# Performance work log

Hardware: AMD Instinct MI355X
Metric: run time of the kernel (lower is better)

## Reference

```python
import jax, jax.numpy as jnp
import numpy as np

B, T, C, H, L, V = 8, 512, 512, 8, 2, 512
DH = C // H
SCALE = 1.0 / np.sqrt(DH)


def _ln(x, g, b):
    mu = jnp.mean(x, -1, keepdims=True)
    var = jnp.mean((x - mu) ** 2, -1, keepdims=True)
    return (x - mu) * jax.lax.rsqrt(var + 1e-5) * g + b


def setup_inputs() -> dict:
    key = jax.random.key(0)
    ks = jax.random.split(key, 16)
    f = lambda k, shape: jax.random.normal(k, shape, jnp.float32) * 0.02
    return {
        "idx": jax.random.randint(ks[0], (B, T), 0, 4),
        "tok_emb": f(ks[1], (4, C)),
        "pos_emb": f(ks[2], (T, C)),
        "ln1_g": jnp.ones((L, C)), "ln1_b": jnp.zeros((L, C)),
        "Wq": f(ks[3], (L, C, C)), "bq": jnp.zeros((L, C)),
        "Wk": f(ks[4], (L, C, C)), "bk": jnp.zeros((L, C)),
        "Wv": f(ks[5], (L, C, C)), "bv": jnp.zeros((L, C)),
        "Wp": f(ks[6], (L, C, C)), "bp": jnp.zeros((L, C)),
        "ln2_g": jnp.ones((L, C)), "ln2_b": jnp.zeros((L, C)),
        "W1": f(ks[7], (L, C, 4 * C)), "b1": jnp.zeros((L, 4 * C)),
        "W2": f(ks[8], (L, 4 * C, C)), "b2": jnp.zeros((L, C)),
        "lnf_g": jnp.ones((C,)), "lnf_b": jnp.zeros((C,)),
        "Whead": f(ks[9], (C, V)),
        "steps": 4,
    }


def _block(x, p):
    (l1g, l1b, wq, bq, wk, bk, wv, bv, wp, bp,
     l2g, l2b, w1, b1, w2, b2) = p
    # attention (mask buffer is all ones in the original -> full attention)
    xn = _ln(x, l1g, l1b)
    q = (xn @ wq + bq).reshape(B, T, H, DH)
    k = (xn @ wk + bk).reshape(B, T, H, DH)
    v = (xn @ wv + bv).reshape(B, T, H, DH)
    att = jnp.einsum('bqhd,bkhd->bhqk', q, k) * SCALE
    att = jax.nn.softmax(att, axis=-1)
    y = jnp.einsum('bhqk,bkhd->bqhd', att, v).reshape(B, T, C)
    x = x + y @ wp + bp
    # MLP with exact (erf) GELU, matching torch nn.GELU default
    h = jax.nn.gelu(_ln(x, l2g, l2b) @ w1 + b1, approximate=False)
    return x + h @ w2 + b2


def reference(idx, tok_emb, pos_emb, ln1_g, ln1_b, Wq, bq, Wk, bk, Wv, bv,
              Wp, bp, ln2_g, ln2_b, W1, b1, W2, b2, lnf_g, lnf_b, Whead,
              steps):
    params = (ln1_g, ln1_b, Wq, bq, Wk, bk, Wv, bv, Wp, bp,
              ln2_g, ln2_b, W1, b1, W2, b2)
    x = tok_emb[idx] + pos_emb[None, :, :]

    def run_blocks(x):
        def step(x, p):
            return _block(x, p), None
        x, _ = jax.lax.scan(step, x, params)
        return x

    for _ in range(steps):  # recurrent application of the whole stack
        x = run_blocks(x)
    x = _ln(x, lnf_g, lnf_b)
    return x @ Whead  # logits [B, T, V]
```

## Files before the change

kernel.cpp:

```cpp
#include <hip/hip_runtime.h>
#include <hip/hip_bf16.h>
#include <math.h>

#define BB 8
#define TT 512
#define CC 512
#define HH 8
#define DH 64
#define LL 2
#define VV 512
#define NSTEPS 4
#define BT (BB*TT)
#define FF (4*CC)

typedef unsigned short u16;
typedef __bf16 bf16x8 __attribute__((ext_vector_type(8)));
typedef float f32x4 __attribute__((ext_vector_type(4)));
typedef u16 u16x8 __attribute__((ext_vector_type(8)));

static __device__ __forceinline__ u16 f2bf(float f) {
    unsigned int u = __float_as_uint(f);
    unsigned int r = (u + 0x7fffu + ((u >> 16) & 1u)) >> 16;
    return (u16)r;
}

static __device__ __forceinline__ void async16(const void* g, void* l) {
    __builtin_amdgcn_global_load_lds((__attribute__((address_space(1))) void*)g,
                                     (__attribute__((address_space(3))) void*)l, 16, 0, 0);
}

static __device__ __forceinline__ int swzp(int r) { return (r ^ (r >> 2)) & 7; }

__global__ void embed_kernel(const int* __restrict__ idx, const float* __restrict__ tok,
                             const float* __restrict__ pos, float* __restrict__ x) {
    int bt = blockIdx.x;
    int t  = threadIdx.x;
    int token = idx[bt];
    int posrow = bt % TT;
    x[(size_t)bt*CC + t]       = tok[token*CC + t]       + pos[posrow*CC + t];
    x[(size_t)bt*CC + t + 256] = tok[token*CC + t + 256] + pos[posrow*CC + t + 256];
}

__global__ __launch_bounds__(256)
void ln_kernel(const float* __restrict__ x, const float* __restrict__ g,
               const float* __restrict__ b, u16* __restrict__ out) {
    int wid = threadIdx.x >> 6, lane = threadIdx.x & 63;
    int row = blockIdx.x * 4 + wid;
    const float* xr = x + (size_t)row * CC;
    f32x4 v0 = ((const f32x4*)xr)[lane*2];
    f32x4 v1 = ((const f32x4*)xr)[lane*2 + 1];
    float s = 0.f, sq = 0.f;
#pragma unroll
    for (int j = 0; j < 4; j++) {
        s += v0[j] + v1[j];
        sq += v0[j]*v0[j] + v1[j]*v1[j];
    }
#pragma unroll
    for (int off = 1; off < 64; off <<= 1) { s += __shfl_xor(s, off); sq += __shfl_xor(sq, off); }
    float mean = s * (1.0f / CC);
    float var  = sq * (1.0f / CC) - mean * mean;
    float inv  = rsqrtf(var + 1e-5f);
    f32x4 g0 = ((const f32x4*)g)[lane*2], g1 = ((const f32x4*)g)[lane*2 + 1];
    f32x4 b0 = ((const f32x4*)b)[lane*2], b1 = ((const f32x4*)b)[lane*2 + 1];
    u16x8 o;
#pragma unroll
    for (int j = 0; j < 4; j++) o[j]     = f2bf((v0[j] - mean) * inv * g0[j] + b0[j]);
#pragma unroll
    for (int j = 0; j < 4; j++) o[4 + j] = f2bf((v1[j] - mean) * inv * g1[j] + b1[j]);
    *(u16x8*)&out[(size_t)row*CC + lane*8] = o;
}

__global__ __launch_bounds__(256)
void cast_all_kernel(const float* __restrict__ Wq, const float* __restrict__ Wk,
                     const float* __restrict__ Wv, const float* __restrict__ Wp,
                     const float* __restrict__ W1, const float* __restrict__ W2,
                     const float* __restrict__ Wh,
                     u16* w_qkvt, u16* w_pt, u16* w_1t, u16* w_2t, u16* w_ht) {
    int bid = blockIdx.x;
    const float* src; u16* dst; int K, N, i0, j0;
    const size_t wcc = (size_t)CC*CC, wcf = (size_t)CC*FF;
    if (bid < 1536) {
        int l = bid / 768, r = bid % 768;
        if (r < 256) {
            int m = r / 64, t = r % 64;
            K = CC; N = CC;
            i0 = (t / 8) * 64; j0 = (t % 8) * 64;
            if      (m == 0) { src = Wq + l*wcc; dst = w_qkvt + (size_t)l*3*wcc; }
            else if (m == 1) { src = Wk + l*wcc; dst = w_qkvt + (size_t)l*3*wcc + wcc; }
            else if (m == 2) { src = Wv + l*wcc; dst = w_qkvt + (size_t)l*3*wcc + 2*wcc; }
            else             { src = Wp + l*wcc; dst = w_pt + (size_t)l*wcc; }
        } else if (r < 512) {
            int t = r - 256;
            K = CC; N = FF;
            i0 = (t / 32) * 64; j0 = (t % 32) * 64;
            src = W1 + l*wcf; dst = w_1t + (size_t)l*wcf;
        } else {
            int t = r - 512;
            K = FF; N = CC;
            i0 = (t / 8) * 64; j0 = (t % 8) * 64;
            src = W2 + l*wcf; dst = w_2t + (size_t)l*wcf;
        }
    } else {
        int t = bid - 1536;
        K = CC; N = CC;
        i0 = (t / 8) * 64; j0 = (t % 8) * 64;
        src = Wh; dst = w_ht;
    }
    __shared__ float tile[64][65];
    int tt = threadIdx.x;
    int rr = tt >> 2, cg = (tt & 3) * 16;
#pragma unroll
    for (int i = 0; i < 16; i++)
        tile[rr][cg + i] = src[(size_t)(i0 + rr) * N + j0 + cg + i];
    __syncthreads();
#pragma unroll
    for (int i = 0; i < 16; i++)
        dst[(size_t)(j0 + rr) * K + i0 + cg + i] = f2bf(tile[cg + i][rr]);
}

template<int BM, int BN, int THREADS, int WROWS, int WCOLS, int EPI>
__global__ __launch_bounds__(THREADS, 6)
void gemm_bt_kernel(const u16* __restrict__ A, const u16* __restrict__ Bt,
                    int N, int K,
                    const float* __restrict__ bias, const float* __restrict__ biask,
                    const float* __restrict__ biasv,
                    float* outf, u16* outq, u16* outk, u16* outvt) {
    constexpr int WTM = BM / WROWS, WTN = BN / WCOLS;
    constexpr int TM = WTM / 16, TN = WTN / 16;
    static_assert(THREADS / 4 == 2 * BM, "A staged in exactly one call");
    static_assert(THREADS == WROWS * WCOLS * 64, "wave grid");
    __shared__ u16 lds_a[2][2][BM][32];
    __shared__ u16 lds_b[2][2][BN][32];
    int tid = threadIdx.x;
    int wid = tid >> 6, lane = tid & 63;
    int quad = lane >> 4, l15 = lane & 15;
    int wm = (wid % WROWS) * WTM, wn = (wid / WROWS) * WTN;

    int NBN = N / BN;
    int lin = blockIdx.x;
    int x8 = lin & 7, slot = lin >> 3;
    int bn = slot % NBN;
    int bm = (slot / NBN) * 8 + x8;

    const int fr = tid >> 2;
    const int c2 = tid & 3;
    const size_t a0 = (size_t)bm * BM, b0 = (size_t)bn * BN;

    auto stage = [&](int buf, int kt) {
        {
            int ks2 = fr / BM, row = fr % BM;
            int g = (ks2 * 4 + c2) ^ swzp(row);
            async16(&A[(a0 + row) * K + kt + g * 8], &lds_a[buf][ks2][row][c2 * 8]);
        }
#pragma unroll
        for (int i = 0; i < (2 * BN) / (THREADS / 4); i++) {
            int f = fr + i * (THREADS / 4);
            int ks2 = f / BN, row = f % BN;
            int g = (ks2 * 4 + c2) ^ swzp(row);
            async16(&Bt[(b0 + row) * K + kt + g * 8], &lds_b[buf][ks2][row][c2 * 8]);
        }
    };

    f32x4 zero = {0.f, 0.f, 0.f, 0.f};
    f32x4 acc[TM][TN];
#pragma unroll
    for (int mi = 0; mi < TM; mi++)
#pragma unroll
        for (int ni = 0; ni < TN; ni++) acc[mi][ni] = zero;

    stage(0, 0);
    __syncthreads();
    const int NKT = K / 64;
    for (int kt = 0; kt < NKT; kt++) {
        int cur = kt & 1;
        if (kt + 1 < NKT) stage(cur ^ 1, (kt + 1) * 64);
#pragma unroll
        for (int ks = 0; ks < 2; ks++) {
            bf16x8 af[TM], bfr[TN];
#pragma unroll
            for (int mi = 0; mi < TM; mi++) {
                int row = wm + mi*16 + l15;
                int lc = (ks*4 + quad) ^ swzp(row);
                af[mi] = *(const bf16x8*)&lds_a[cur][lc >> 2][row][(lc & 3) * 8];
            }
#pragma unroll
            for (int ni = 0; ni < TN; ni++) {
                int row = wn + ni*16 + l15;
                int lc = (ks*4 + quad) ^ swzp(row);
                bfr[ni] = *(const bf16x8*)&lds_b[cur][lc >> 2][row][(lc & 3) * 8];
            }
#pragma unroll
            for (int mi = 0; mi < TM; mi++)
#pragma unroll
                for (int ni = 0; ni < TN; ni++)
                    acc[mi][ni] = __builtin_amdgcn_mfma_f32_16x16x32_bf16(af[mi], bfr[ni], acc[mi][ni], 0, 0, 0);
        }
        __syncthreads();
    }

#pragma unroll
    for (int mi = 0; mi < TM; mi++)
#pragma unroll
        for (int ni = 0; ni < TN; ni++)
#pragma unroll
            for (int i = 0; i < 4; i++) {
                int row = bm*BM + wm + mi*16 + quad*4 + i;
                int col = bn*BN + wn + ni*16 + l15;
                float v = acc[mi][ni][i];
                if (EPI == 0) {
                    int region = col >> 9, cl = col & 511;
                    if (region == 0) {
                        v = (v + bias[cl]) * 0.125f;
                        outq[(size_t)row*512 + cl] = f2bf(v);
                    } else if (region == 1) {
                        v += biask[cl];
                        outk[(size_t)row*512 + cl] = f2bf(v);
                    } else {
                        v += biasv[cl];
                        int bb = row >> 9, tpos = row & 511, hh = cl >> 6, dh = cl & 63;
                        outvt[(((size_t)(bb*8 + hh)*64 + dh) << 9) + tpos] = f2bf(v);
                    }
                } else if (EPI == 1) {
                    size_t idx2 = (size_t)row * N + col;
                    v += bias[col] + outf[idx2];
                    outf[idx2] = v;
                } else if (EPI == 2) {
                    v += bias[col];
                    v = 0.5f * v * (1.0f + erff(v * 0.70710678118654752f));
                    outq[(size_t)row * N + col] = f2bf(v);
                } else {
                    outf[(size_t)row * N + col] = v;
                }
            }
}

__global__ __launch_bounds__(256)
void attn_mfma_kernel(const u16* __restrict__ q, const u16* __restrict__ k,
                      const u16* __restrict__ vt, u16* __restrict__ y) {
    __shared__ u16 lq[64][64];
    __shared__ u16 lk[2][64][64];
    __shared__ u16 lv[2][64][64];
    __shared__ u16 lp[4][16][72];
    int qt = blockIdx.x, h = blockIdx.y, b = blockIdx.z;
    int tid = threadIdx.x;
    int wid = tid >> 6, lane = tid & 63;
    int quad = lane >> 4, l15 = lane & 15;
    const int sr = tid >> 3;
    const int sc = (tid & 7) * 8;
    const int gsc = (((tid & 7) ^ swzp(sr)) << 3);

    auto stageKV = [&](int buf, int kt) {
#pragma unroll
        for (int c = 0; c < 2; c++) {
            async16(&k[(size_t)(b*TT + kt*64 + c*32 + sr)*CC + h*DH + gsc], &lk[buf][c*32 + sr][sc]);
            async16(&vt[((size_t)((b*HH + h)*DH + c*32 + sr))*TT + kt*64 + gsc], &lv[buf][c*32 + sr][sc]);
        }
    };

#pragma unroll
    for (int c = 0; c < 2; c++)
        async16(&q[(size_t)(b*TT + qt*64 + c*32 + sr)*CC + h*DH + gsc], &lq[c*32 + sr][sc]);
    stageKV(0, 0);
    __syncthreads();

    f32x4 zero = {0.f, 0.f, 0.f, 0.f};
    f32x4 acc_o[4];
    float m_st[4], l_st[4];
#pragma unroll
    for (int i = 0; i < 4; i++) { m_st[i] = -INFINITY; l_st[i] = 0.f; }
#pragma unroll
    for (int ni = 0; ni < 4; ni++) acc_o[ni] = zero;

    const int rowq = wid*16 + l15;
    const int pq = swzp(rowq);

    for (int kt = 0; kt < TT/64; kt++) {
        int cur = kt & 1;
        if (kt + 1 < TT/64) stageKV(cur ^ 1, kt + 1);

        f32x4 s[4];
#pragma unroll
        for (int ni = 0; ni < 4; ni++) s[ni] = zero;
#pragma unroll
        for (int ks = 0; ks < 2; ks++) {
            int lcq = (ks*4 + quad) ^ pq;
            bf16x8 aq = *(const bf16x8*)&lq[rowq][lcq * 8];
            bf16x8 bfr[4];
#pragma unroll
            for (int ni = 0; ni < 4; ni++) {
                int rowk = ni*16 + l15;
                int lck = (ks*4 + quad) ^ swzp(rowk);
                bfr[ni] = *(const bf16x8*)&lk[cur][rowk][lck * 8];
            }
#pragma unroll
            for (int ni = 0; ni < 4; ni++)
                s[ni] = __builtin_amdgcn_mfma_f32_16x16x32_bf16(aq, bfr[ni], s[ni], 0, 0, 0);
        }

#pragma unroll
        for (int i = 0; i < 4; i++) {
            float mx = -INFINITY;
#pragma unroll
            for (int ni = 0; ni < 4; ni++) mx = fmaxf(mx, s[ni][i]);
#pragma unroll
            for (int off = 1; off < 16; off <<= 1) mx = fmaxf(mx, __shfl_xor(mx, off));
            float mn = fmaxf(m_st[i], mx);
            float al = __expf(m_st[i] - mn);
            float rs = 0.f;
#pragma unroll
            for (int ni = 0; ni < 4; ni++) {
                float p = __expf(s[ni][i] - mn);
                s[ni][i] = p;
                rs += p;
            }
#pragma unroll
            for (int off = 1; off < 16; off <<= 1) rs += __shfl_xor(rs, off);
            l_st[i] = l_st[i] * al + rs;
            m_st[i] = mn;
#pragma unroll
            for (int ni = 0; ni < 4; ni++) acc_o[ni][i] *= al;
        }

#pragma unroll
        for (int ni = 0; ni < 4; ni++)
#pragma unroll
            for (int i = 0; i < 4; i++)
                lp[wid][quad*4 + i][ni*16 + l15] = f2bf(s[ni][i]);

#pragma unroll
        for (int ks = 0; ks < 2; ks++) {
            bf16x8 pa = *(const bf16x8*)&lp[wid][l15][ks*32 + quad*8];
            bf16x8 vb[4];
#pragma unroll
            for (int ni = 0; ni < 4; ni++) {
                int rowv = ni*16 + l15;
                int lcv = (ks*4 + quad) ^ swzp(rowv);
                vb[ni] = *(const bf16x8*)&lv[cur][rowv][lcv * 8];
            }
#pragma unroll
            for (int ni = 0; ni < 4; ni++)
                acc_o[ni] = __builtin_amdgcn_mfma_f32_16x16x32_bf16(pa, vb[ni], acc_o[ni], 0, 0, 0);
        }
        __syncthreads();
    }

#pragma unroll
    for (int i = 0; i < 4; i++) {
        float inv = 1.0f / l_st[i];
#pragma unroll
        for (int ni = 0; ni < 4; ni++) {
            int qrow = qt*64 + wid*16 + quad*4 + i;
            int col  = h*DH + ni*16 + l15;
            y[(size_t)(b*TT + qrow)*CC + col] = f2bf(acc_o[ni][i] * inv);
        }
    }
}

extern "C" void kernel_launch(void* const* d_in, const int* in_sizes, int n_in,
                              void* d_out, int out_size, void* d_ws, size_t ws_size,
                              hipStream_t stream) {
    const int*   idx   = (const int*)d_in[0];
    const float* tok   = (const float*)d_in[1];
    const float* pos   = (const float*)d_in[2];
    const float* ln1g  = (const float*)d_in[3];
    const float* ln1b  = (const float*)d_in[4];
    const float* Wq    = (const float*)d_in[5];
    const float* bq    = (const float*)d_in[6];
    const float* Wk    = (const float*)d_in[7];
    const float* bk    = (const float*)d_in[8];
    const float* Wv    = (const float*)d_in[9];
    const float* bv    = (const float*)d_in[10];
    const float* Wp    = (const float*)d_in[11];
    const float* bp    = (const float*)d_in[12];
    const float* ln2g  = (const float*)d_in[13];
    const float* ln2b  = (const float*)d_in[14];
    const float* W1    = (const float*)d_in[15];
    const float* b1    = (const float*)d_in[16];
    const float* W2    = (const float*)d_in[17];
    const float* b2    = (const float*)d_in[18];
    const float* lnfg  = (const float*)d_in[19];
    const float* lnfb  = (const float*)d_in[20];
    const float* Whead = (const float*)d_in[21];

    float* x  = (float*)d_ws;
    u16* xn   = (u16*)(x + (size_t)BT*CC);
    u16* R    = xn + (size_t)BT*CC;
    u16* qb   = R;
    u16* kb   = R + (size_t)BT*CC;
    u16* vtb  = R + (size_t)2*BT*CC;
    u16* hb   = R;
    u16* w_qkvt = R + (size_t)4*BT*CC;
    u16* w_pt   = w_qkvt + (size_t)2*3*CC*CC;
    u16* w_1t   = w_pt   + (size_t)2*CC*CC;
    u16* w_2t   = w_1t   + (size_t)2*CC*FF;
    u16* w_ht   = w_2t   + (size_t)2*FF*CC;

    cast_all_kernel<<<1600, 256, 0, stream>>>(Wq, Wk, Wv, Wp, W1, W2, Whead,
                                              w_qkvt, w_pt, w_1t, w_2t, w_ht);
    embed_kernel<<<BT, 256, 0, stream>>>(idx, tok, pos, x);

    const int g_qkv  = (3*CC/128) * (BT/64);
    const int g_fc1  = (FF/128)   * (BT/64);
    const int g_proj = (CC/64)    * (BT/32);
    const int g_fc2  = (CC/64)    * (BT/32);
    const int g_head = (VV/64)    * (BT/32);

    for (int s = 0; s < NSTEPS; s++) {
        for (int l = 0; l < LL; l++) {
            ln_kernel<<<BT/4, 256, 0, stream>>>(x, ln1g + l*CC, ln1b + l*CC, xn);
            gemm_bt_kernel<64,128,512,2,4,0><<<g_qkv, 512, 0, stream>>>(
                xn, w_qkvt + (size_t)l*3*CC*CC, 3*CC, CC,
                bq + l*CC, bk + l*CC, bv + l*CC, nullptr, qb, kb, vtb);
            attn_mfma_kernel<<<dim3(TT/64, HH, BB), 256, 0, stream>>>(qb, kb, vtb, xn);
            gemm_bt_kernel<32,64,256,2,2,1><<<g_proj, 256, 0, stream>>>(
                xn, w_pt + (size_t)l*CC*CC, CC, CC,
                bp + l*CC, nullptr, nullptr, x, nullptr, nullptr, nullptr);
            ln_kernel<<<BT/4, 256, 0, stream>>>(x, ln2g + l*CC, ln2b + l*CC, xn);
            gemm_bt_kernel<64,128,512,2,4,2><<<g_fc1, 512, 0, stream>>>(
                xn, w_1t + (size_t)l*CC*FF, FF, CC,
                b1 + (size_t)l*FF, nullptr, nullptr, nullptr, hb, nullptr, nullptr);
            gemm_bt_kernel<32,64,256,2,2,1><<<g_fc2, 256, 0, stream>>>(
                hb, w_2t + (size_t)l*FF*CC, CC, FF,
                b2 + l*CC, nullptr, nullptr, x, nullptr, nullptr, nullptr);
        }
    }

    ln_kernel<<<BT/4, 256, 0, stream>>>(x, lnfg, lnfb, xn);
    gemm_bt_kernel<32,64,256,2,2,3><<<g_head, 256, 0, stream>>>(
        xn, w_ht, VV, CC, nullptr, nullptr, nullptr, (float*)d_out, nullptr, nullptr, nullptr);
}
```

Measured before the change: 916.9 us.

## Load GEMM MFMA fragments directly from global memory, drop LDS staging

Removes the LDS double-buffered async staging from the GEMM kernel. Each wave now loads its bf16 MFMA fragments straight from global memory into registers, ping-ponging two register sets across 32-wide k slices. Tile and wave shapes change (256 threads, wider N tiles for the proj, fc2 and head GEMMs), and the occupancy hint is dropped. This removes LDS traffic and barriers, but data is no longer shared between waves through LDS, so global and L2 traffic rises and the row-strided loads may coalesce poorly.

```diff
diff --git a/kernel.cpp b/kernel.cpp
--- a/kernel.cpp
+++ b/kernel.cpp
@@ -118,8 +118,8 @@
         dst[(size_t)(j0 + rr) * K + i0 + cg + i] = f2bf(tile[cg + i][rr]);
 }
 
-template<int BM, int BN, int THREADS, int WROWS, int WCOLS, int EPI>
-__global__ __launch_bounds__(THREADS, 6)
+template<int BM, int BN, int WROWS, int WCOLS, int EPI>
+__global__ __launch_bounds__(WROWS*WCOLS*64)
 void gemm_bt_kernel(const u16* __restrict__ A, const u16* __restrict__ Bt,
                     int N, int K,
                     const float* __restrict__ bias, const float* __restrict__ biask,
@@ -127,10 +127,6 @@
                     float* outf, u16* outq, u16* outk, u16* outvt) {
     constexpr int WTM = BM / WROWS, WTN = BN / WCOLS;
     constexpr int TM = WTM / 16, TN = WTN / 16;
-    static_assert(THREADS / 4 == 2 * BM, "A staged in exactly one call");
-    static_assert(THREADS == WROWS * WCOLS * 64, "wave grid");
-    __shared__ u16 lds_a[2][2][BM][32];
-    __shared__ u16 lds_b[2][2][BN][32];
     int tid = threadIdx.x;
     int wid = tid >> 6, lane = tid & 63;
     int quad = lane >> 4, l15 = lane & 15;
@@ -142,24 +138,9 @@
     int bn = slot % NBN;
     int bm = (slot / NBN) * 8 + x8;
 
-    const int fr = tid >> 2;
-    const int c2 = tid & 3;
     const size_t a0 = (size_t)bm * BM, b0 = (size_t)bn * BN;
-
-    auto stage = [&](int buf, int kt) {
-        {
-            int ks2 = fr / BM, row = fr % BM;
-            int g = (ks2 * 4 + c2) ^ swzp(row);
-            async16(&A[(a0 + row) * K + kt + g * 8], &lds_a[buf][ks2][row][c2 * 8]);
-        }
-#pragma unroll
-        for (int i = 0; i < (2 * BN) / (THREADS / 4); i++) {
-            int f = fr + i * (THREADS / 4);
-            int ks2 = f / BN, row = f % BN;
-            int g = (ks2 * 4 + c2) ^ swzp(row);
-            async16(&Bt[(b0 + row) * K + kt + g * 8], &lds_b[buf][ks2][row][c2 * 8]);
-        }
-    };
+    const u16* Abase = A  + (a0 + wm + l15) * (size_t)K + quad * 8;
+    const u16* Bbase = Bt + (b0 + wn + l15) * (size_t)K + quad * 8;
 
     f32x4 zero = {0.f, 0.f, 0.f, 0.f};
     f32x4 acc[TM][TN];
@@ -168,34 +149,29 @@
 #pragma unroll
         for (int ni = 0; ni < TN; ni++) acc[mi][ni] = zero;
 
-    stage(0, 0);
-    __syncthreads();
-    const int NKT = K / 64;
-    for (int kt = 0; kt < NKT; kt++) {
-        int cur = kt & 1;
-        if (kt + 1 < NKT) stage(cur ^ 1, (kt + 1) * 64);
-#pragma unroll
-        for (int ks = 0; ks < 2; ks++) {
-            bf16x8 af[TM], bfr[TN];
-#pragma unroll
-            for (int mi = 0; mi < TM; mi++) {
-                int row = wm + mi*16 + l15;
-                int lc = (ks*4 + quad) ^ swzp(row);
-                af[mi] = *(const bf16x8*)&lds_a[cur][lc >> 2][row][(lc & 3) * 8];
-            }
-#pragma unroll
-            for (int ni = 0; ni < TN; ni++) {
-                int row = wn + ni*16 + l15;
-                int lc = (ks*4 + quad) ^ swzp(row);
-                bfr[ni] = *(const bf16x8*)&lds_b[cur][lc >> 2][row][(lc & 3) * 8];
-            }
-#pragma unroll
-            for (int mi = 0; mi < TM; mi++)
-#pragma unroll
-                for (int ni = 0; ni < TN; ni++)
-                    acc[mi][ni] = __builtin_amdgcn_mfma_f32_16x16x32_bf16(af[mi], bfr[ni], acc[mi][ni], 0, 0, 0);
-        }
-        __syncthreads();
+    bf16x8 afA[TM], bfA[TN], afB[TM], bfB[TN];
+    auto loadf = [&](bf16x8* af, bf16x8* bf, int kt) {
+#pragma unroll
+        for (int mi = 0; mi < TM; mi++)
+            af[mi] = *(const bf16x8*)(Abase + (size_t)mi * 16 * K + kt);
+#pragma unroll
+        for (int ni = 0; ni < TN; ni++)
+            bf[ni] = *(const bf16x8*)(Bbase + (size_t)ni * 16 * K + kt);
+    };
+    auto domfma = [&](bf16x8* af, bf16x8* bf) {
+#pragma unroll
+        for (int mi = 0; mi < TM; mi++)
+#pragma unroll
+            for (int ni = 0; ni < TN; ni++)
+                acc[mi][ni] = __builtin_amdgcn_mfma_f32_16x16x32_bf16(af[mi], bf[ni], acc[mi][ni], 0, 0, 0);
+    };
+
+    loadf(afA, bfA, 0);
+    for (int kt = 0; kt < K; kt += 64) {
+        loadf(afB, bfB, kt + 32);
+        domfma(afA, bfA);
+        if (kt + 64 < K) loadf(afA, bfA, kt + 64);
+        domfma(afB, bfB);
     }
 
 #pragma unroll
@@ -401,31 +377,31 @@
 
     const int g_qkv  = (3*CC/128) * (BT/64);
     const int g_fc1  = (FF/128)   * (BT/64);
-    const int g_proj = (CC/64)    * (BT/32);
-    const int g_fc2  = (CC/64)    * (BT/32);
-    const int g_head = (VV/64)    * (BT/32);
+    const int g_proj = (CC/128)   * (BT/32);
+    const int g_fc2  = (CC/128)   * (BT/32);
+    const int g_head = (VV/128)   * (BT/32);
 
     for (int s = 0; s < NSTEPS; s++) {
         for (int l = 0; l < LL; l++) {
             ln_kernel<<<BT/4, 256, 0, stream>>>(x, ln1g + l*CC, ln1b + l*CC, xn);
-            gemm_bt_kernel<64,128,512,2,4,0><<<g_qkv, 512, 0, stream>>>(
+            gemm_bt_kernel<64,128,2,2,0><<<g_qkv, 256, 0, stream>>>(
                 xn, w_qkvt + (size_t)l*3*CC*CC, 3*CC, CC,
                 bq + l*CC, bk + l*CC, bv + l*CC, nullptr, qb, kb, vtb);
             attn_mfma_kernel<<<dim3(TT/64, HH, BB), 256, 0, stream>>>(qb, kb, vtb, xn);
-            gemm_bt_kernel<32,64,256,2,2,1><<<g_proj, 256, 0, stream>>>(
+            gemm_bt_kernel<32,128,1,4,1><<<g_proj, 256, 0, stream>>>(
                 xn, w_pt + (size_t)l*CC*CC, CC, CC,
                 bp + l*CC, nullptr, nullptr, x, nullptr, nullptr, nullptr);
             ln_kernel<<<BT/4, 256, 0, stream>>>(x, ln2g + l*CC, ln2b + l*CC, xn);
-            gemm_bt_kernel<64,128,512,2,4,2><<<g_fc1, 512, 0, stream>>>(
+            gemm_bt_kernel<64,128,2,2,2><<<g_fc1, 256, 0, stream>>>(
                 xn, w_1t + (size_t)l*CC*FF, FF, CC,
                 b1 + (size_t)l*FF, nullptr, nullptr, nullptr, hb, nullptr, nullptr);
-            gemm_bt_kernel<32,64,256,2,2,1><<<g_fc2, 256, 0, stream>>>(
+            gemm_bt_kernel<32,128,1,4,1><<<g_fc2, 256, 0, stream>>>(
                 hb, w_2t + (size_t)l*FF*CC, CC, FF,
                 b2 + l*CC, nullptr, nullptr, x, nullptr, nullptr, nullptr);
         }
     }
 
     ln_kernel<<<BT/4, 256, 0, stream>>>(x, lnfg, lnfb, xn);
-    gemm_bt_kernel<32,64,256,2,2,3><<<g_head, 256, 0, stream>>>(
+    gemm_bt_kernel<32,128,1,4,3><<<g_head, 256, 0, stream>>>(
         xn, w_ht, VV, CC, nullptr, nullptr, nullptr, (float*)d_out, nullptr, nullptr, nullptr);
 }
```

Measured after the change: 1.771 ms. +93.1%, slower.
